# Performance work log

Measured on AMD Instinct MI355X. Metric: run time of the kernel, lower is better.

The kernel has to match this reference:

```python
import jax, jax.numpy as jnp
import numpy as np

# matcher cost weights (init_kwargs)
W_CLASS, W_3DCENTER, W_BBOX, W_GIOU = 2.0, 10.0, 5.0, 2.0
ALPHA, GAMMA, EPS = 0.25, 2.0, 1e-8


def _box_cxcylrtb_to_xyxy(b):
    # (cx, cy, l, r, t, b) -> (x1, y1, x2, y2)
    cx, cy, l, r, t, bo = (b[..., i] for i in range(6))
    return jnp.stack([cx - l, cy - t, cx + r, cy + bo], axis=-1)


def _generalized_box_iou(b1, b2):
    # b1 [N,4], b2 [M,4] in xyxy -> GIoU matrix [N,M]
    area1 = (b1[:, 2] - b1[:, 0]) * (b1[:, 3] - b1[:, 1])
    area2 = (b2[:, 2] - b2[:, 0]) * (b2[:, 3] - b2[:, 1])
    lt = jnp.maximum(b1[:, None, :2], b2[None, :, :2])
    rb = jnp.minimum(b1[:, None, 2:], b2[None, :, 2:])
    wh = jnp.clip(rb - lt, 0.0)
    inter = wh[..., 0] * wh[..., 1]
    union = area1[:, None] + area2[None, :] - inter
    iou = inter / union
    lt_e = jnp.minimum(b1[:, None, :2], b2[None, :, :2])
    rb_e = jnp.maximum(b1[:, None, 2:], b2[None, :, 2:])
    wh_e = jnp.clip(rb_e - lt_e, 0.0)
    area_e = wh_e[..., 0] * wh_e[..., 1]
    return iou - (area_e - union) / area_e


def _l1_cdist(a, b):
    return jnp.abs(a[:, None, :] - b[None, :, :]).sum(-1)


def _cost_matrix(pred_logits, pred_boxes, tgt_labels, tgt_boxes):
    bs, nq, _ = pred_boxes.shape
    out_prob = jax.nn.sigmoid(pred_logits.reshape(bs * nq, -1))
    tgt_ids = tgt_labels.reshape(-1)
    neg = (1.0 - ALPHA) * out_prob ** GAMMA * -jnp.log(1.0 - out_prob + EPS)
    pos = ALPHA * (1.0 - out_prob) ** GAMMA * -jnp.log(out_prob + EPS)
    cost_class = (pos - neg)[:, tgt_ids]              # [bs*nq, bs*nt]
    out_flat = pred_boxes.reshape(bs * nq, 6)
    tgt_flat = tgt_boxes.reshape(-1, 6)
    cost_3dcenter = _l1_cdist(out_flat[:, 0:2], tgt_flat[:, 0:2])
    cost_bbox = _l1_cdist(out_flat[:, 2:6], tgt_flat[:, 2:6])
    cost_giou = -_generalized_box_iou(_box_cxcylrtb_to_xyxy(out_flat), _box_cxcylrtb_to_xyxy(tgt_flat))
    C = W_BBOX * cost_bbox + W_3DCENTER * cost_3dcenter + W_CLASS * cost_class + W_GIOU * cost_giou
    return C.reshape(bs, nq, -1)


def _lsa(cost):
    # Rectangular linear sum assignment (Jonker-Volgenant / e-maxx Hungarian),
    # scipy.optimize.linear_sum_assignment compatible (row-sorted output).
    cost = np.asarray(cost, dtype=np.float64)
    transposed = cost.shape[0] > cost.shape[1]
    if transposed:
        cost = cost.T
    n, m = cost.shape  # n <= m
    u = np.zeros(n + 1)
    v = np.zeros(m + 1)
    p = np.zeros(m + 1, dtype=np.int64)    # p[j] = row matched to col j (1-indexed)
    way = np.zeros(m + 1, dtype=np.int64)
    INF = np.inf
    for i in range(1, n + 1):
        p[0] = i
        j0 = 0
        minv = np.full(m + 1, INF)
        used = np.zeros(m + 1, dtype=bool)
        while True:
            used[j0] = True
            i0 = p[j0]
            free = ~used[1:]
            cur = cost[i0 - 1, :] - u[i0] - v[1:]
            upd = free & (cur < minv[1:])
            minv[1:][upd] = cur[upd]
            way[1:][upd] = j0
            cand = np.where(free, minv[1:], INF)
            j1 = int(np.argmin(cand)) + 1
            delta = cand[j1 - 1]
            u[p[used]] += delta
            v[used] -= delta
            minv[~used] -= delta
            j0 = j1
            if p[j0] == 0:
                break
        while j0 != 0:
            j1 = way[j0]
            p[j0] = p[j1]
            j0 = j1
    cols = np.nonzero(p[1:])[0]
    rows = p[1:][cols] - 1
    if transposed:
        rows, cols = cols, rows
    order = np.argsort(rows)
    return rows[order], cols[order]


def _assign(Cn, nt, group_num):
    # per-sample block-diagonal cost slicing + per-group Hungarian, like the torch loop
    bs, nq, _ = Cn.shape
    g_nq = nq // group_num
    pred_idx, tgt_idx = [], []
    for b in range(bs):
        Cb = Cn[b, :, b * nt:(b + 1) * nt]
        rows, cols = [], []
        for g in range(group_num):
            r, c = _lsa(Cb[g * g_nq:(g + 1) * g_nq])
            rows.append(r + g * g_nq)
            cols.append(c)
        pred_idx.append(np.concatenate(rows))
        tgt_idx.append(np.concatenate(cols))
    return np.stack(pred_idx), np.stack(tgt_idx)


def setup_inputs() -> dict:
    key = jax.random.key(0)
    k1, k2, k3, k4 = jax.random.split(key, 4)
    bs, nq, nc, nt = 16, 550, 91, 48
    return {
        "pred_logits": jax.random.normal(k1, (bs, nq, nc), jnp.float32),
        "pred_boxes": jax.random.uniform(k2, (bs, nq, 6), jnp.float32),
        "tgt_labels": jax.random.randint(k3, (bs, nt), 0, nc),
        "tgt_boxes": jax.random.uniform(k4, (bs, nt, 6), jnp.float32),
        "group_num": 11,
    }


def reference(pred_logits, pred_boxes, tgt_labels, tgt_boxes, group_num):
    C = _cost_matrix(pred_logits, pred_boxes, tgt_labels, tgt_boxes)  # [bs, nq, bs*nt]
    nt = tgt_boxes.shape[1]
    Cn = np.asarray(jax.device_get(C), dtype=np.float64)
    pi, ti = _assign(Cn, nt, int(group_num))
    return C, jnp.asarray(pi), jnp.asarray(ti)
```

## Files before the change

kernel.cpp:

```cpp
#include <hip/hip_runtime.h>
#include <math.h>

#define BS 16
#define NQ 550
#define NC 91
#define NT 48
#define GN 11
#define GQ 50
#define NTOT (BS * NT)
#define NROW 48
#define MCOL 50
#define NPAIR (GN * NT)
#define NLSA (BS * GN)

__device__ __forceinline__ float focal_cost_f32(float x) {
    float prob = 1.0f / (1.0f + __expf(-x));
    float q = 1.0f - prob;
    float lneg = __logf(q + 1e-8f);
    float lpos = __logf(prob + 1e-8f);
    float neg = 0.75f * (prob * prob) * (-lneg);
    float pos = 0.25f * (q * q) * (-lpos);
    return pos - neg;
}

__device__ __forceinline__ float cost_element(
    const float* __restrict__ logits,
    const float* __restrict__ pboxes, const int* __restrict__ labels,
    const float* __restrict__ tboxes, int p, int t)
{
    const float* pb = pboxes + (long)p * 6;
    float pcx = pb[0], pcy = pb[1], pl = pb[2], pr = pb[3], ptt = pb[4], pbo = pb[5];
    const float* tb = tboxes + (long)t * 6;
    float tcx = tb[0], tcy = tb[1], tl = tb[2], tr = tb[3], ttt = tb[4], tbo = tb[5];

    float c3d = __fadd_rn(fabsf(__fsub_rn(pcx, tcx)), fabsf(__fsub_rn(pcy, tcy)));
    float cbb = __fadd_rn(
                  __fadd_rn(
                    __fadd_rn(fabsf(__fsub_rn(pl, tl)), fabsf(__fsub_rn(pr, tr))),
                    fabsf(__fsub_rn(ptt, ttt))),
                  fabsf(__fsub_rn(pbo, tbo)));

    float px1 = __fsub_rn(pcx, pl), py1 = __fsub_rn(pcy, ptt);
    float px2 = __fadd_rn(pcx, pr), py2 = __fadd_rn(pcy, pbo);
    float tx1 = __fsub_rn(tcx, tl), ty1 = __fsub_rn(tcy, ttt);
    float tx2 = __fadd_rn(tcx, tr), ty2 = __fadd_rn(tcy, tbo);

    float area1 = __fmul_rn(__fsub_rn(px2, px1), __fsub_rn(py2, py1));
    float area2 = __fmul_rn(__fsub_rn(tx2, tx1), __fsub_rn(ty2, ty1));
    float ltx = fmaxf(px1, tx1), lty = fmaxf(py1, ty1);
    float rbx = fminf(px2, tx2), rby = fminf(py2, ty2);
    float wx = fmaxf(__fsub_rn(rbx, ltx), 0.0f);
    float wy = fmaxf(__fsub_rn(rby, lty), 0.0f);
    float inter = __fmul_rn(wx, wy);
    float uni = __fsub_rn(__fadd_rn(area1, area2), inter);
    float iou = __fdiv_rn(inter, uni);
    float ex1 = fminf(px1, tx1), ey1 = fminf(py1, ty1);
    float ex2 = fmaxf(px2, tx2), ey2 = fmaxf(py2, ty2);
    float ew = fmaxf(__fsub_rn(ex2, ex1), 0.0f);
    float eh = fmaxf(__fsub_rn(ey2, ey1), 0.0f);
    float earea = __fmul_rn(ew, eh);
    float giou = __fsub_rn(iou, __fdiv_rn(__fsub_rn(earea, uni), earea));
    float cgiou = -giou;

    float cclass = focal_cost_f32(logits[(long)p * NC + labels[t]]);

    float out = __fmul_rn(5.0f, cbb);
    out = __fadd_rn(out, __fmul_rn(10.0f, c3d));
    out = __fadd_rn(out, __fmul_rn(2.0f, cclass));
    out = __fadd_rn(out, __fmul_rn(2.0f, cgiou));
    return out;
}

__device__ __forceinline__ double readlane_f64(double x, int l) {
    long long b = __double_as_longlong(x);
    int lo = __builtin_amdgcn_readlane((int)(b & 0xffffffffLL), l);
    int hi = __builtin_amdgcn_readlane((int)(b >> 32), l);
    return __longlong_as_double(((long long)hi << 32) | (unsigned int)lo);
}

template <int CTRL, int RM>
__device__ __forceinline__ float dpp_min_f32(float x) {
    int xi = __float_as_int(x);
    int t = __builtin_amdgcn_update_dpp(xi, xi, CTRL, RM, 0xf, false);
    return fminf(x, __int_as_float(t));
}

__device__ __forceinline__ float wave_min_key(float v) {
    float r = v;
    r = dpp_min_f32<0x111, 0xf>(r);
    r = dpp_min_f32<0x112, 0xf>(r);
    r = dpp_min_f32<0x114, 0xf>(r);
    r = dpp_min_f32<0x118, 0xf>(r);
    r = dpp_min_f32<0x142, 0xa>(r);
    r = dpp_min_f32<0x143, 0xc>(r);
    return __int_as_float(__builtin_amdgcn_readlane(__float_as_int(r), 63));
}

__global__ __launch_bounds__(256) void mega_kernel(
    const float* __restrict__ logits,
    const float* __restrict__ pboxes,
    const int*   __restrict__ labels,
    const float* __restrict__ tboxes,
    float*       __restrict__ C,
    float*       __restrict__ pi,
    float*       __restrict__ ti)
{
    if (blockIdx.x >= NLSA) {
        long idx = (long)(blockIdx.x - NLSA) * 256 + threadIdx.x;
        if (idx >= (long)BS * NQ * NTOT) return;
        int t = (int)(idx % NTOT);
        int p = (int)(idx / NTOT);
        C[idx] = cost_element(logits, pboxes, labels, tboxes, p, t);
        return;
    }

    const int blk = blockIdx.x;
    const int b = blk / GN, g = blk % GN;
    const int tid = threadIdx.x;

    __shared__ double lcost[NROW * MCOL];

    for (int k = tid; k < NROW * MCOL; k += 256) {
        int i = k % NROW, j = k / NROW;
        float cf = cost_element(logits, pboxes, labels, tboxes,
                                b * NQ + g * GQ + j, b * NT + i);
        lcost[i * MCOL + j] = (double)cf;
    }
    __syncthreads();
    if (tid >= 64) return;

    const int lane = tid;
    const bool incol = (lane >= 1 && lane <= MCOL);
    const int cidx = incol ? lane - 1 : 0;
    const double INF = __builtin_inf();
    const float INFF = __builtin_inff();

    int    pcol_l = 0;
    double urow_l = 0.0;
    double v_l    = 0.0;
    int    way_l  = 0;
    double minv_l = INF;
    float  kprev  = INFF;
    bool   used_l = false;

    for (int i = 1; i <= NROW; ++i) {
        if (lane == 0) { pcol_l = i; urow_l = 0.0; }
        minv_l = INF;
        kprev  = INFF;
        used_l = false;
        int j0 = 0;
        int i0 = i;
        double u_i0 = 0.0;
        double cd = lcost[(i0 - 1) * MCOL + cidx];

        for (int guard = 0; guard <= MCOL + 1; ++guard) {
            used_l = used_l || (lane == j0);
            bool freel = incol && !used_l;

            double cur = (cd - u_i0) - v_l;
            bool upd   = freel && (cur < minv_l);
            minv_l = upd ? cur : minv_l;
            way_l  = upd ? j0  : way_l;

            float kf = freel ? fminf(__double2float_rn(cur), kprev) : INFF;

            float kmin = wave_min_key(kf);
            unsigned long long mm = __ballot(kf == kmin);
            int j1 = (int)__builtin_ctzll(mm);

            int    i0n   = __builtin_amdgcn_readlane(pcol_l, j1);
            double delta = readlane_f64(minv_l, j1);
            double u_nx  = readlane_f64(urow_l, j1);

            int r_next = (i0n > 0) ? (i0n - 1) : 0;
            double cd_next = lcost[r_next * MCOL + cidx];

            urow_l = used_l ? urow_l + delta : urow_l;
            v_l    = used_l ? v_l - delta    : v_l;
            minv_l = freel  ? minv_l - delta : minv_l;
            kprev  = __double2float_rn(minv_l);

            j0 = j1;
            if (i0n == 0) break;
            i0   = i0n;
            u_i0 = u_nx;
            cd   = cd_next;
        }

        int j = j0;
        while (j != 0) {
            int wj    = __builtin_amdgcn_readlane(way_l, j);
            int pr    = __builtin_amdgcn_readlane(pcol_l, wj);
            double ur = readlane_f64(urow_l, wj);
            if (lane == j) { pcol_l = pr; urow_l = ur; }
            j = wj;
        }
    }

    unsigned long long asg = __ballot(incol && pcol_l != 0);
    if (incol && pcol_l != 0) {
        int k = __popcll(asg & ((1ull << lane) - 1));
        float* pib = pi + ((long)b * NPAIR + (long)g * NT);
        float* tib = ti + ((long)b * NPAIR + (long)g * NT);
        pib[k] = (float)(g * GQ + cidx);
        tib[k] = (float)(pcol_l - 1);
    }
}

extern "C" void kernel_launch(void* const* d_in, const int* in_sizes, int n_in,
                              void* d_out, int out_size, void* d_ws, size_t ws_size,
                              hipStream_t stream) {
    const float* logits = (const float*)d_in[0];
    const float* pboxes = (const float*)d_in[1];
    const int*   labels = (const int*)d_in[2];
    const float* tboxes = (const float*)d_in[3];

    float* out = (float*)d_out;
    float* C  = out;
    float* pi = out + (long)BS * NQ * NTOT;
    float* ti = pi + (long)BS * NPAIR;

    long total = (long)BS * NQ * NTOT;
    int cost_blocks = (int)((total + 255) / 256);
    int mega_blocks = NLSA + cost_blocks;

    mega_kernel<<<mega_blocks, 256, 0, stream>>>(
        logits, pboxes, labels, tboxes, C, pi, ti);
}
```

Baseline: 170.3 us.

## Defer Hungarian dual updates using cumulative delta offsets

Reworks the inner Dijkstra-style Hungarian step so the per-iteration dual updates (urow, v, minv adjustments by delta) are no longer applied every step. The code now tracks a running dsum and a per-column snapshot taken when each column becomes used, then applies the accumulated adjustment once after the augmenting path is found. This removes several double-precision select and adds from the serial critical loop. In exchange it changes floating-point rounding order, which can alter tie-breaking relative to the reference.

```diff
diff --git a/kernel.cpp b/kernel.cpp
--- a/kernel.cpp
+++ b/kernel.cpp
@@ -139,52 +139,51 @@
     double urow_l = 0.0;
     double v_l    = 0.0;
     int    way_l  = 0;
-    double minv_l = INF;
-    float  kprev  = INFF;
-    bool   used_l = false;
 
     for (int i = 1; i <= NROW; ++i) {
         if (lane == 0) { pcol_l = i; urow_l = 0.0; }
-        minv_l = INF;
-        kprev  = INFF;
-        used_l = false;
-        int j0 = 0;
-        int i0 = i;
-        double u_i0 = 0.0;
-        double cd = lcost[(i0 - 1) * MCOL + cidx];
+
+        double mraw_l  = INF;
+        bool   used_l  = false;
+        double dused_l = 0.0;
+        double dsum    = 0.0;
+        int    j0 = 0;
+        double cdu = lcost[(i - 1) * MCOL + cidx];
 
         for (int guard = 0; guard <= MCOL + 1; ++guard) {
-            used_l = used_l || (lane == j0);
+            bool newly = (lane == j0) && !used_l;
+            dused_l = newly ? dsum : dused_l;
+            used_l  = used_l || (lane == j0);
             bool freel = incol && !used_l;
 
-            double cur = (cd - u_i0) - v_l;
-            bool upd   = freel && (cur < minv_l);
-            minv_l = upd ? cur : minv_l;
+            double m_in = (cdu - v_l) + dsum;
+            bool upd   = freel && (m_in < mraw_l);
+            mraw_l = upd ? m_in : mraw_l;
             way_l  = upd ? j0  : way_l;
 
-            float kf = freel ? fminf(__double2float_rn(cur), kprev) : INFF;
+            float kf = freel ? __double2float_rn(mraw_l - dsum) : INFF;
 
             float kmin = wave_min_key(kf);
             unsigned long long mm = __ballot(kf == kmin);
             int j1 = (int)__builtin_ctzll(mm);
 
-            int    i0n   = __builtin_amdgcn_readlane(pcol_l, j1);
-            double delta = readlane_f64(minv_l, j1);
-            double u_nx  = readlane_f64(urow_l, j1);
+            int    i0n    = __builtin_amdgcn_readlane(pcol_l, j1);
+            double dsum_n = readlane_f64(mraw_l, j1);
+            double u_nx   = readlane_f64(urow_l, j1);
 
             int r_next = (i0n > 0) ? (i0n - 1) : 0;
             double cd_next = lcost[r_next * MCOL + cidx];
 
-            urow_l = used_l ? urow_l + delta : urow_l;
-            v_l    = used_l ? v_l - delta    : v_l;
-            minv_l = freel  ? minv_l - delta : minv_l;
-            kprev  = __double2float_rn(minv_l);
-
+            dsum = dsum_n;
             j0 = j1;
             if (i0n == 0) break;
-            i0   = i0n;
-            u_i0 = u_nx;
-            cd   = cd_next;
+            cdu = cd_next - u_nx;
+        }
+
+        {
+            double adj = dsum - dused_l;
+            v_l    = used_l ? v_l - adj    : v_l;
+            urow_l = used_l ? urow_l + adj : urow_l;
         }
 
         int j = j0;
```

Result: slower. 183.4 us (+7.7%).
